# Performance work log

Measured on AMD Instinct MI355X. Metric: run time of the kernel, lower is better.

The kernel has to match this reference:

```python
import jax, jax.numpy as jnp
import numpy as np

KSIZE = 3  # kernel_size from init_kwargs


def _unfold_same(x, ks):
    """Torch nn.Unfold with fixed 'same' padding. x:(B,C,H,W) -> (B, C*ks*ks, H, W).
    Channel ordering matches torch unfold: (c, kh, kw) with c outermost."""
    B, C, H, W = x.shape
    pad_total = ks - 1
    pb = pad_total // 2
    pe = pad_total - pb
    xp = jnp.pad(x, ((0, 0), (0, 0), (pb, pe), (pb, pe)))
    # small fixed loop over ks*ks = 9 taps
    patches = jnp.stack(
        [xp[:, :, di:di + H, dj:dj + W] for di in range(ks) for dj in range(ks)],
        axis=2,
    )  # (B, C, ks*ks, H, W)
    return patches.reshape(B, C * ks * ks, H, W)


def setup_inputs() -> dict:
    key = jax.random.key(0)
    k1, k2 = jax.random.split(key)
    B, C, H, W = 16, 32, 256, 256
    O, ks = 64, KSIZE
    K = C * ks * ks  # 288
    x = jax.random.normal(k1, (B, C, H, W), dtype=jnp.float32)
    limit = float(np.sqrt(6.0 / (K + O)))  # xavier_uniform
    weight = jax.random.uniform(k2, (O, K), jnp.float32, -limit, limit)
    bias = jnp.zeros((O, 1), dtype=jnp.float32)
    return {"x": x, "weight": weight, "bias": bias}


def reference(x, weight, bias):
    # Faithful math of Linear.forward: same-padded unfold, then per-pixel
    # out[n,o] = sum_k weight[o,k] * patch[n,k] + bias[o], reshaped to (B,O,H,W).
    # Expressed as a single contraction instead of the (N,O,K) broadcast intermediate.
    patches = _unfold_same(x, KSIZE)                     # (B, K, H, W)
    out = jnp.einsum('ok,bkhw->bohw', weight, patches)   # (B, O, H, W)
    out = out + bias.reshape(1, -1, 1, 1)
    return out
```

## Files before the change

### kernel.cpp

```cpp
#include <hip/hip_runtime.h>
#include <hip/hip_bf16.h>

#define CIN 32
#define OCH 64
#define HH  256
#define WW  256
#define HW  (HH * WW)
#define BH  8
#define ROWB (258 * CIN * 2)

typedef __bf16 bf16x8 __attribute__((ext_vector_type(8)));
typedef float  f32x4  __attribute__((ext_vector_type(4)));

__global__ __launch_bounds__(256, 2) void conv_fused_kernel(
        const float* __restrict__ x, const float* __restrict__ wgt,
        const float* __restrict__ bias, float* __restrict__ out) {
    const int bid = blockIdx.x;
    const int nid = (bid & 7) * 64 + (bid >> 3);
    const int b   = nid >> 5;
    const int h0  = (nid & 31) * BH;
    const int tid = threadIdx.x;
    const int l   = tid & 63, wid = tid >> 6;
    const int lm  = l & 15,  lh  = l >> 4;

    __shared__ __bf16 xs[4][258][CIN];
    char* lds = (char*)&xs[0][0][0];
    const float* xb = x + (size_t)b * CIN * HW;

    if (tid < 32) {
        const int s = tid >> 3, k = tid & 7;
        const int wp = (k < 4) ? 0 : 257;
        *(f32x4*)(lds + s * ROWB + wp * 64 + (k & 3) * 16) = (f32x4){0, 0, 0, 0};
    }

    bf16x8 af[9];
    {
        const float* wp_ = wgt + (size_t)(wid * 16 + lm) * 288 + (size_t)lh * 8 * 9;
#pragma unroll
        for (int t = 0; t < 9; ++t)
#pragma unroll
            for (int j = 0; j < 8; ++j)
                af[t][j] = (__bf16)wp_[j * 9 + t];
    }
    float bv[4];
#pragma unroll
    for (int r = 0; r < 4; ++r) bv[r] = bias[wid * 16 + lh * 4 + r];

    auto stage = [&](int row) {
        char* slot = lds + ((row + 1) & 3) * ROWB;
        if (row >= 0 && row < HH) {
            const float* rp = xb + (size_t)row * WW;
#pragma unroll
            for (int wh = 0; wh < 2; ++wh) {
                float2 v[8];
#pragma unroll
                for (int j = 0; j < 8; ++j)
                    v[j] = *(const float2*)(rp + (size_t)(wid * 8 + j) * HW + wh * 128 + 2 * l);
#pragma unroll
                for (int p = 0; p < 2; ++p) {
                    const int w = wh * 128 + 2 * l + p;
                    bf16x8 pk;
#pragma unroll
                    for (int j = 0; j < 8; ++j) pk[j] = (__bf16)(p ? v[j].y : v[j].x);
                    *(bf16x8*)(slot + (w + 1) * 64 + ((wid ^ ((w >> 1) & 3)) << 4)) = pk;
                }
            }
        } else {
#pragma unroll
            for (int wh = 0; wh < 2; ++wh)
#pragma unroll
                for (int p = 0; p < 2; ++p) {
                    const int w = wh * 128 + 2 * l + p;
                    *(f32x4*)(slot + (w + 1) * 64 + ((wid ^ ((w >> 1) & 3)) << 4)) =
                        (f32x4){0, 0, 0, 0};
                }
        }
    };

    stage(h0 - 1); stage(h0); stage(h0 + 1);

    int off[3];
#pragma unroll
    for (int kw = 0; kw < 3; ++kw) {
        const int u = lm + kw - 1;
        const int m = (u < 0) ? 3 : ((u >> 1) & 3);
        off[kw] = (lm + kw) * 64 + ((lh ^ m) << 4);
    }

    __syncthreads();

    for (int i = 0; i < BH; ++i) {
        const int h  = h0 + i;
        const int nr = h + 2;
        const bool ldnext = (i < BH - 1) && (nr < HH);
        const bool zrnext = (i < BH - 1) && (nr >= HH);

        float2 v[16];
        if (ldnext) {
            const float* rp = xb + (size_t)nr * WW;
#pragma unroll
            for (int wh = 0; wh < 2; ++wh)
#pragma unroll
                for (int j = 0; j < 8; ++j)
                    v[wh * 8 + j] =
                        *(const float2*)(rp + (size_t)(wid * 8 + j) * HW + wh * 128 + 2 * l);
        }

        const char* base[3] = { lds + ((h    ) & 3) * ROWB,
                                lds + ((h + 1) & 3) * ROWB,
                                lds + ((h + 2) & 3) * ROWB };
        f32x4 acc[16];
#pragma unroll
        for (int nt = 0; nt < 16; ++nt) acc[nt] = (f32x4){0, 0, 0, 0};
#pragma unroll
        for (int nt = 0; nt < 16; ++nt)
#pragma unroll
            for (int kh = 0; kh < 3; ++kh)
#pragma unroll
                for (int kw = 0; kw < 3; ++kw) {
                    bf16x8 bf = *(const bf16x8*)(base[kh] + off[kw] + nt * 1024);
                    acc[nt] = __builtin_amdgcn_mfma_f32_16x16x32_bf16(
                        af[kh * 3 + kw], bf, acc[nt], 0, 0, 0);
                }

        float* outb = out + (size_t)b * OCH * HW + (size_t)h * WW;
#pragma unroll
        for (int nt = 0; nt < 16; ++nt)
#pragma unroll
            for (int r2 = 0; r2 < 4; ++r2)
                outb[(size_t)(wid * 16 + lh * 4 + r2) * HW + nt * 16 + lm] =
                    acc[nt][r2] + bv[r2];

        if (ldnext) {
            char* slot = lds + ((nr + 1) & 3) * ROWB;
#pragma unroll
            for (int wh = 0; wh < 2; ++wh)
#pragma unroll
                for (int p = 0; p < 2; ++p) {
                    const int w = wh * 128 + 2 * l + p;
                    bf16x8 pk;
#pragma unroll
                    for (int j = 0; j < 8; ++j)
                        pk[j] = (__bf16)(p ? v[wh * 8 + j].y : v[wh * 8 + j].x);
                    *(bf16x8*)(slot + (w + 1) * 64 + ((wid ^ ((w >> 1) & 3)) << 4)) = pk;
                }
        } else if (zrnext) {
            char* slot = lds + ((nr + 1) & 3) * ROWB;
#pragma unroll
            for (int wh = 0; wh < 2; ++wh)
#pragma unroll
                for (int p = 0; p < 2; ++p) {
                    const int w = wh * 128 + 2 * l + p;
                    *(f32x4*)(slot + (w + 1) * 64 + ((wid ^ ((w >> 1) & 3)) << 4)) =
                        (f32x4){0, 0, 0, 0};
                }
        }
        __syncthreads();
    }
}

extern "C" void kernel_launch(void* const* d_in, const int* in_sizes, int n_in,
                              void* d_out, int out_size, void* d_ws, size_t ws_size,
                              hipStream_t stream) {
    const float* x    = (const float*)d_in[0];
    const float* w    = (const float*)d_in[1];
    const float* bias = (const float*)d_in[2];
    float* out = (float*)d_out;

    hipLaunchKernelGGL(conv_fused_kernel, dim3(16 * (HH / BH)), dim3(256), 0, stream,
                       x, w, bias, out);
}
```

Before: 109.3 us.

## Rewrite conv as per-wave 32-wide tiles with 32x32 MFMA and private LDS rings

Each wave now owns a 32-column by 8-row output tile for 32 output channels, keeping its own small LDS ring buffer of input rows with halo columns. Because no other wave shares the ring, block-wide barriers are gone. It switches from 16x16x32 to 32x32x16 bf16 MFMA and double-buffers the next row in registers so global loads overlap compute. It raises occupancy to 3 blocks per SM and launches 2048 blocks. Input rows are now loaded twice, once by each wave of a channel-group pair, and the extra halo loads add redundant traffic.

```diff
diff --git a/kernel.cpp b/kernel.cpp
--- a/kernel.cpp
+++ b/kernel.cpp
@@ -7,155 +7,137 @@
 #define WW  256
 #define HW  (HH * WW)
 #define BH  8
-#define ROWB (258 * CIN * 2)
+#define SLOTB (34 * 64)
+#define RINGB (4 * SLOTB)
 
 typedef __bf16 bf16x8 __attribute__((ext_vector_type(8)));
-typedef float  f32x4  __attribute__((ext_vector_type(4)));
+typedef float  f32x16 __attribute__((ext_vector_type(16)));
 
-__global__ __launch_bounds__(256, 2) void conv_fused_kernel(
+__global__ __launch_bounds__(256, 3) void conv_wave_kernel(
         const float* __restrict__ x, const float* __restrict__ wgt,
         const float* __restrict__ bias, float* __restrict__ out) {
     const int bid = blockIdx.x;
-    const int nid = (bid & 7) * 64 + (bid >> 3);
-    const int b   = nid >> 5;
-    const int h0  = (nid & 31) * BH;
+    const int nid = (bid & 7) * 256 + (bid >> 3);
     const int tid = threadIdx.x;
-    const int l   = tid & 63, wid = tid >> 6;
-    const int lm  = l & 15,  lh  = l >> 4;
+    const int wid = tid >> 6, l = tid & 63;
+    const int unit = nid * 2 + (wid >> 1);
+    const int og = wid & 1;
+    const int wt = unit & 7;
+    const int ht = (unit >> 3) & 31;
+    const int b  = unit >> 8;
+    const int w0 = wt * 32;
+    const int h0 = ht * BH;
+    const int lw = l & 31;
+    const int hi = l >> 5;
 
-    __shared__ __bf16 xs[4][258][CIN];
-    char* lds = (char*)&xs[0][0][0];
+    __shared__ char lds_all[4][RINGB];
+    char* ring = &lds_all[wid][0];
     const float* xb = x + (size_t)b * CIN * HW;
 
-    if (tid < 32) {
-        const int s = tid >> 3, k = tid & 7;
-        const int wp = (k < 4) ? 0 : 257;
-        *(f32x4*)(lds + s * ROWB + wp * 64 + (k & 3) * 16) = (f32x4){0, 0, 0, 0};
+    bf16x8 af[9][2];
+    {
+        const float* wrow = wgt + (size_t)(og * 32 + lw) * 288 + hi * 8 * 9;
+#pragma unroll
+        for (int ks = 0; ks < 2; ++ks)
+#pragma unroll
+            for (int t = 0; t < 9; ++t)
+#pragma unroll
+                for (int j = 0; j < 8; ++j)
+                    af[t][ks][j] = (__bf16)wrow[ks * 144 + j * 9 + t];
     }
 
-    bf16x8 af[9];
-    {
-        const float* wp_ = wgt + (size_t)(wid * 16 + lm) * 288 + (size_t)lh * 8 * 9;
-#pragma unroll
-        for (int t = 0; t < 9; ++t)
-#pragma unroll
-            for (int j = 0; j < 8; ++j)
-                af[t][j] = (__bf16)wp_[j * 9 + t];
-    }
-    float bv[4];
-#pragma unroll
-    for (int r = 0; r < 4; ++r) bv[r] = bias[wid * 16 + lh * 4 + r];
+    const int wp  = (l & 15) * 2;
+    const int g   = l >> 4;
+    const int wgh = w0 + (hi ? 32 : -1);
+    const int chh = lw;
 
-    auto stage = [&](int row) {
-        char* slot = lds + ((row + 1) & 3) * ROWB;
+    auto loadrow = [&](int row, float2 (&v)[8], float& hv) {
         if (row >= 0 && row < HH) {
             const float* rp = xb + (size_t)row * WW;
 #pragma unroll
-            for (int wh = 0; wh < 2; ++wh) {
-                float2 v[8];
-#pragma unroll
-                for (int j = 0; j < 8; ++j)
-                    v[j] = *(const float2*)(rp + (size_t)(wid * 8 + j) * HW + wh * 128 + 2 * l);
-#pragma unroll
-                for (int p = 0; p < 2; ++p) {
-                    const int w = wh * 128 + 2 * l + p;
-                    bf16x8 pk;
-#pragma unroll
-                    for (int j = 0; j < 8; ++j) pk[j] = (__bf16)(p ? v[j].y : v[j].x);
-                    *(bf16x8*)(slot + (w + 1) * 64 + ((wid ^ ((w >> 1) & 3)) << 4)) = pk;
-                }
-            }
+            for (int j = 0; j < 8; ++j)
+                v[j] = *(const float2*)(rp + (size_t)(g * 8 + j) * HW + w0 + wp);
+            hv = (wgh >= 0 && wgh < WW) ? rp[(size_t)chh * HW + wgh] : 0.f;
         } else {
 #pragma unroll
-            for (int wh = 0; wh < 2; ++wh)
-#pragma unroll
-                for (int p = 0; p < 2; ++p) {
-                    const int w = wh * 128 + 2 * l + p;
-                    *(f32x4*)(slot + (w + 1) * 64 + ((wid ^ ((w >> 1) & 3)) << 4)) =
-                        (f32x4){0, 0, 0, 0};
-                }
+            for (int j = 0; j < 8; ++j) v[j] = make_float2(0.f, 0.f);
+            hv = 0.f;
         }
     };
 
-    stage(h0 - 1); stage(h0); stage(h0 + 1);
+    auto writerow = [&](int row, float2 (&v)[8], float hv) {
+        char* slot = ring + ((row + 1) & 3) * SLOTB;
+#pragma unroll
+        for (int p = 0; p < 2; ++p) {
+            const int wl = wp + p;
+            const int wglob = w0 + wl;
+            bf16x8 pk;
+#pragma unroll
+            for (int j = 0; j < 8; ++j) pk[j] = (__bf16)(p ? v[j].y : v[j].x);
+            *(bf16x8*)(slot + (wl + 1) * 64 + ((g ^ ((wglob >> 1) & 3)) << 4)) = pk;
+        }
+        const int e  = hi ? 33 : 0;
+        const int mh = (wgh < 0) ? 3 : ((wgh >> 1) & 3);
+        *(__bf16*)(slot + e * 64 + (((chh >> 3) ^ mh) << 4) + (chh & 7) * 2) =
+            (__bf16)hv;
+    };
 
-    int off[3];
+    {
+        float2 t0[8]; float th;
+        loadrow(h0 - 1, t0, th); writerow(h0 - 1, t0, th);
+        loadrow(h0,     t0, th); writerow(h0,     t0, th);
+        loadrow(h0 + 1, t0, th); writerow(h0 + 1, t0, th);
+    }
+    float2 vA[8], vB[8]; float hA = 0.f, hB = 0.f;
+    loadrow(h0 + 2, vA, hA);
+
+    int off6[3][2];
 #pragma unroll
     for (int kw = 0; kw < 3; ++kw) {
-        const int u = lm + kw - 1;
+        const int u = w0 + lw + kw - 1;
         const int m = (u < 0) ? 3 : ((u >> 1) & 3);
-        off[kw] = (lm + kw) * 64 + ((lh ^ m) << 4);
+#pragma unroll
+        for (int ks = 0; ks < 2; ++ks)
+            off6[kw][ks] = (lw + kw) * 64 + (((ks * 2 + hi) ^ m) << 4);
     }
 
-    __syncthreads();
+    const float* bp = bias + og * 32 + 4 * hi;
+    float* ob = out + ((size_t)b * OCH + og * 32) * HW + (size_t)h0 * WW + w0 + lw;
 
-    for (int i = 0; i < BH; ++i) {
-        const int h  = h0 + i;
-        const int nr = h + 2;
-        const bool ldnext = (i < BH - 1) && (nr < HH);
-        const bool zrnext = (i < BH - 1) && (nr >= HH);
+    auto body = [&](int i, float2 (&vprev)[8], float hprev,
+                    float2 (&vnext)[8], float& hnext) {
+        const int h = h0 + i;
+        if (i < 6) loadrow(h + 3, vnext, hnext);
 
-        float2 v[16];
-        if (ldnext) {
-            const float* rp = xb + (size_t)nr * WW;
+        f32x16 acc;
 #pragma unroll
-            for (int wh = 0; wh < 2; ++wh)
+        for (int r = 0; r < 16; ++r) acc[r] = 0.f;
 #pragma unroll
-                for (int j = 0; j < 8; ++j)
-                    v[wh * 8 + j] =
-                        *(const float2*)(rp + (size_t)(wid * 8 + j) * HW + wh * 128 + 2 * l);
+        for (int kh = 0; kh < 3; ++kh) {
+            const char* s = ring + ((h + kh) & 3) * SLOTB;
+#pragma unroll
+            for (int ks = 0; ks < 2; ++ks)
+#pragma unroll
+                for (int kw = 0; kw < 3; ++kw) {
+                    bf16x8 bf = *(const bf16x8*)(s + off6[kw][ks]);
+                    acc = __builtin_amdgcn_mfma_f32_32x32x16_bf16(
+                        af[kh * 3 + kw][ks], bf, acc, 0, 0, 0);
+                }
         }
 
-        const char* base[3] = { lds + ((h    ) & 3) * ROWB,
-                                lds + ((h + 1) & 3) * ROWB,
-                                lds + ((h + 2) & 3) * ROWB };
-        f32x4 acc[16];
+        if (i < 7) writerow(h + 2, vprev, hprev);
+
+        float* obr = ob + (size_t)i * WW;
 #pragma unroll
-        for (int nt = 0; nt < 16; ++nt) acc[nt] = (f32x4){0, 0, 0, 0};
-#pragma unroll
-        for (int nt = 0; nt < 16; ++nt)
-#pragma unroll
-            for (int kh = 0; kh < 3; ++kh)
-#pragma unroll
-                for (int kw = 0; kw < 3; ++kw) {
-                    bf16x8 bf = *(const bf16x8*)(base[kh] + off[kw] + nt * 1024);
-                    acc[nt] = __builtin_amdgcn_mfma_f32_16x16x32_bf16(
-                        af[kh * 3 + kw], bf, acc[nt], 0, 0, 0);
-                }
+        for (int r = 0; r < 16; ++r) {
+            const int ro = (r & 3) + 8 * (r >> 2);
+            obr[(size_t)(ro + 4 * hi) * HW] = acc[r] + bp[ro];
+        }
+    };
 
-        float* outb = out + (size_t)b * OCH * HW + (size_t)h * WW;
-#pragma unroll
-        for (int nt = 0; nt < 16; ++nt)
-#pragma unroll
-            for (int r2 = 0; r2 < 4; ++r2)
-                outb[(size_t)(wid * 16 + lh * 4 + r2) * HW + nt * 16 + lm] =
-                    acc[nt][r2] + bv[r2];
-
-        if (ldnext) {
-            char* slot = lds + ((nr + 1) & 3) * ROWB;
-#pragma unroll
-            for (int wh = 0; wh < 2; ++wh)
-#pragma unroll
-                for (int p = 0; p < 2; ++p) {
-                    const int w = wh * 128 + 2 * l + p;
-                    bf16x8 pk;
-#pragma unroll
-                    for (int j = 0; j < 8; ++j)
-                        pk[j] = (__bf16)(p ? v[wh * 8 + j].y : v[wh * 8 + j].x);
-                    *(bf16x8*)(slot + (w + 1) * 64 + ((wid ^ ((w >> 1) & 3)) << 4)) = pk;
-                }
-        } else if (zrnext) {
-            char* slot = lds + ((nr + 1) & 3) * ROWB;
-#pragma unroll
-            for (int wh = 0; wh < 2; ++wh)
-#pragma unroll
-                for (int p = 0; p < 2; ++p) {
-                    const int w = wh * 128 + 2 * l + p;
-                    *(f32x4*)(slot + (w + 1) * 64 + ((wid ^ ((w >> 1) & 3)) << 4)) =
-                        (f32x4){0, 0, 0, 0};
-                }
-        }
-        __syncthreads();
+    for (int i2 = 0; i2 < 4; ++i2) {
+        body(i2 * 2,     vA, hA, vB, hB);
+        body(i2 * 2 + 1, vB, hB, vA, hA);
     }
 }
 
@@ -167,6 +149,6 @@
     const float* bias = (const float*)d_in[2];
     float* out = (float*)d_out;
 
-    hipLaunchKernelGGL(conv_fused_kernel, dim3(16 * (HH / BH)), dim3(256), 0, stream,
+    hipLaunchKernelGGL(conv_wave_kernel, dim3(2048), dim3(256), 0, stream,
                        x, w, bias, out);
 }
```

After: 372.7 us. 241% more time.
